# Kernel optimization log

Hardware: AMD Instinct MI355X
Metric: run time of the kernel (lower is better)

The kernel has to match this reference:

```python
import jax, jax.numpy as jnp
import numpy as np

LMAX = 3
MUL = 64


def _build_masks(lmax, mul):
    dim = mul * sum(2 * l + 1 for l in range(lmax + 1))
    masks = np.zeros((lmax + 1, dim), dtype=bool)
    off = 0
    for l in range(lmax + 1):
        base = off + np.arange(mul) * (2 * l + 1) + l
        masks[0, base] = True
        for m in range(1, l + 1):
            masks[m, base + m] = True
            masks[m, base - m] = True
        off += mul * (2 * l + 1)
    idx = [np.nonzero(masks[m])[0] for m in range(lmax + 1)]
    return dim, idx

DIM, IDX = _build_masks(LMAX, MUL)
C_M = [MUL * (LMAX + 1 - m) for m in range(LMAX + 1)]  # 256,192,128,64
WSL = np.cumsum([0] + C_M)  # weight slices per m; weight_numel = 640


def setup_inputs() -> dict:
    E = 65536
    key = jax.random.key(0)
    ks = jax.random.split(key, 16)
    inp = {
        'x': jax.random.normal(ks[0], (E, DIM), jnp.float32),
        'D0': jax.random.normal(ks[1], (E, 1, 1), jnp.float32),
        'D1': jax.random.normal(ks[2], (E, 3, 3), jnp.float32),
        'D2': jax.random.normal(ks[3], (E, 5, 5), jnp.float32),
        'D3': jax.random.normal(ks[4], (E, 7, 7), jnp.float32),
        'weight': jax.random.normal(ks[5], (E, int(WSL[-1])), jnp.float32),
        'mask_edge': jax.random.randint(ks[6], (E,), 0, 2) > 0,
        'W0': jax.random.normal(ks[7], (C_M[0], C_M[0]), jnp.float32) * 0.05,
        'b0': jax.random.normal(ks[8], (C_M[0],), jnp.float32) * 0.05,
        'W1': jax.random.normal(ks[9], (2 * C_M[1], C_M[1]), jnp.float32) * 0.05,
        'W2': jax.random.normal(ks[10], (2 * C_M[2], C_M[2]), jnp.float32) * 0.05,
        'W3': jax.random.normal(ks[11], (2 * C_M[3], C_M[3]), jnp.float32) * 0.05,
    }
    return inp


def _rotate(v, Ds, inverse):
    # per-l block Wigner rotation: [E, mul*(2l+1)] blocks, small batched einsum
    off = 0
    outs = []
    for l in range(LMAX + 1):
        n = 2 * l + 1
        blk = v[:, off:off + MUL * n].reshape(-1, MUL, n)
        if inverse:
            r = jnp.einsum('zcj,zij->zci', blk, Ds[l])
        else:
            r = jnp.einsum('zcj,zji->zci', blk, Ds[l])
        outs.append(r.reshape(-1, MUL * n))
        off += MUL * n
    return jnp.concatenate(outs, axis=-1)


def _so2_forward(x, Ds, weight, mask_edge, W0, b0, Wms):
    x_new = _rotate(x, Ds, inverse=False)
    me = mask_edge.astype(x.dtype)[:, None]
    out = jnp.zeros_like(x_new)  # irreps_out == irreps_in -> same dim
    # m = 0
    x0 = x_new[:, IDX[0]]
    y0 = x0 @ W0.T + b0
    out = out.at[:, IDX[0]].set(y0 * weight[:, WSL[0]:WSL[1]] * me)
    # m > 0
    for m in range(1, LMAX + 1):
        c = C_M[m]
        # gather interleaved (neg, pos) pairs -> [E, 2, c_in]
        xm = x_new[:, IDX[m]].reshape(-1, c, 2).transpose(0, 2, 1)
        y = jnp.einsum('zmc,oc->zmo', xm, Wms[m - 1])  # [E, 2, 2c]
        y_neg = y[:, 0, :c] + y[:, 1, c:]
        y_pos = y[:, 1, :c] - y[:, 0, c:]
        wm = weight[:, WSL[m]:WSL[m + 1]]
        # torch code flattens [neg_all, pos_all] onto ascending masked positions
        vals = jnp.concatenate([y_neg * wm, y_pos * wm], axis=-1) * me
        out = out.at[:, IDX[m]].set(vals)
    return _rotate(out, Ds, inverse=True)


def reference(x, D0, D1, D2, D3, weight, mask_edge, W0, b0, W1, W2, W3):
    return _so2_forward(x, [D0, D1, D2, D3], weight, mask_edge, W0, b0, [W1, W2, W3])
```

## Files before the change

kernel.cpp:

```cpp
#include <hip/hip_runtime.h>
#include <hip/hip_bf16.h>


#define EPB 16
#define BRICK_USHORTS 294912
#define WS_NEED (589824 + 16)

typedef __attribute__((ext_vector_type(8))) short short8v;
typedef __attribute__((ext_vector_type(4))) float float4v;
typedef unsigned short ushort;

__device__ __forceinline__ float bf2f(__hip_bfloat16 v) { return __bfloat162float(v); }
__device__ __forceinline__ ushort f2bb(float v) {
    __hip_bfloat16 h = __float2bfloat16(v);
    return *reinterpret_cast<ushort*>(&h);
}
__device__ __forceinline__ float bb2f(ushort u) {
    __hip_bfloat16 h = *reinterpret_cast<__hip_bfloat16*>(&u);
    return __bfloat162float(h);
}

__device__ int classify_wave(const void* p, int lane)
{
    const unsigned char* b = (const unsigned char*)p;
    bool ok01 = true;
    #pragma unroll
    for (int j = 0; j < 4; ++j) if (b[lane * 4 + j] > 1) ok01 = false;
    if (__all(ok01)) return 0;
    const unsigned* w = (const unsigned*)p;
    const unsigned v = w[lane];
    const unsigned lo = v & 0xFFFFu, hi = v >> 16;
    const bool f32b  = (v == 0u || v == 0x3F800000u);
    const bool bf16b = (lo == 0u || lo == 0x3F80u) && (hi == 0u || hi == 0x3F80u);
    const bool f16b  = (lo == 0u || lo == 0x3C00u) && (hi == 0u || hi == 0x3C00u);
    if (__all(f32b) | __all(bf16b) | __all(f16b)) return 0;
    const float* f = (const float*)p;
    float mx = 0.f;
    #pragma unroll
    for (int j = 0; j < 4; ++j) mx = fmaxf(mx, fabsf(f[lane * 4 + j]));
    #pragma unroll
    for (int d = 1; d < 64; d <<= 1) mx = fmaxf(mx, __shfl_xor(mx, d));
    return (mx < 0.35f) ? 1 : 2;
}

__device__ int detect_stride_wave(const unsigned char* mb, int lane)
{
    unsigned orr[8] = {0,0,0,0,0,0,0,0};
    unsigned maxb = 0, minnz = 255;
    #pragma unroll
    for (int j = 0; j < 16; ++j) {
        unsigned v = mb[lane * 16 + j];
        orr[j & 7] |= v;
        if (v) { maxb = max(maxb, v); minnz = min(minnz, v); }
    }
    #pragma unroll
    for (int d = 1; d < 64; d <<= 1) {
        #pragma unroll
        for (int r = 0; r < 8; ++r) orr[r] |= (unsigned)__shfl_xor((int)orr[r], d);
        maxb  = max(maxb, (unsigned)__shfl_xor((int)maxb, d));
        minnz = min(minnz, (unsigned)__shfl_xor((int)minnz, d));
    }
    const unsigned oddnz = orr[1] | orr[3] | orr[5] | orr[7];
    const bool intbool = (maxb <= 1u) || (maxb == 255u && minnz == 255u);
    if (intbool) {
        if (oddnz)                  return 1;
        else if (orr[2] | orr[6])   return 2;
        else if (orr[4])            return 4;
        else                        return 8;
    } else {
        if (orr[0])                 return 2;
        else if (orr[1])            return 2;
        else if (orr[2])            return 4;
        else                        return 8;
    }
}

__global__ void so2_prep(const void* t0, const void* t1, const void* t2,
                         const float* __restrict__ W1,
                         const float* __restrict__ W2,
                         const float* __restrict__ W3,
                         ushort* __restrict__ Bb)
{
    const int lane = threadIdx.x;
    const int c0 = classify_wave(t0, lane);
    const int c1 = classify_wave(t1, lane);
    const int c2 = classify_wave(t2, lane);
    const void* sel[3];
    int im, id;
    if (c0 != c1 && c0 != c2 && c1 != c2) {
        sel[c0] = t0; sel[c1] = t1; sel[c2] = t2;
        im = (c0 == 0) ? 0 : (c1 == 0) ? 1 : 2;
        id = (c0 == 2) ? 0 : (c1 == 2) ? 1 : 2;
    } else {
        sel[2] = t0; sel[0] = t1; sel[1] = t2;
        im = 1; id = 0;
    }
    const float* sW0 = (const float*)sel[1];
    if (blockIdx.x == 0) {
        const int stride = detect_stride_wave((const unsigned char*)sel[0], lane);
        if (lane == 0) {
            int* hdr = (int*)(Bb + BRICK_USHORTS);
            hdr[0] = im; hdr[1] = id; hdr[2] = stride;
        }
    }

    const int brick = blockIdx.x;
    int m, r, KT;
    if (brick < 128)      { m = 0; r = brick;       KT = 8;  }
    else if (brick < 416) { m = 1; r = brick - 128; KT = 12; }
    else if (brick < 544) { m = 2; r = brick - 416; KT = 8;  }
    else                  { m = 3; r = brick - 544; KT = 4;  }
    const int nt = r / KT, kt = r - nt * KT;
    const float* Wm = (m == 0) ? sW0 : (m == 1) ? W1 : (m == 2) ? W2 : W3;
    const int c = (m == 0) ? 256 : (m == 1) ? 192 : (m == 2) ? 128 : 64;

    const int col = nt * 16 + (lane & 15);
    const int kb  = kt * 32 + (lane >> 4) * 8;
    ushort* dst = Bb + ((size_t)brick << 9) + lane * 8;
    #pragma unroll
    for (int i = 0; i < 8; ++i) {
        const int k = kb + i;
        float v;
        if (m == 0) v = Wm[(size_t)col * 256 + k];
        else if (col < c) v = (k < c) ? Wm[(size_t)col * c + k]
                                      : Wm[(size_t)(c + col) * c + (k - c)];
        else {
            const int o = col - c;
            v = (k < c) ? -Wm[(size_t)(c + o) * c + k]
                        :  Wm[(size_t)o * c + (k - c)];
        }
        dst[i] = f2bb(v);
    }
}

template<int M>
__device__ __forceinline__ void run_unit(
    const ushort (*A_lds)[1024], ushort (*Y_lds)[1024],
    const ushort* __restrict__ Bb,
    const float* __restrict__ weightp, const float* __restrict__ b0,
    const float* me_sh, int e0, int nt, int lane)
{
    constexpr int KT   = (M == 0) ? 8 : (M == 1) ? 12 : (M == 2) ? 8 : 4;
    constexpr int segk = (M == 0) ? 0 : (M == 1) ? 256 : (M == 2) ? 640 : 896;
    constexpr int c    = (M == 0) ? 256 : (M == 1) ? 192 : (M == 2) ? 128 : 64;
    constexpr int wsl  = (M == 0) ? 0 : (M == 1) ? 256 : (M == 2) ? 448 : 576;
    constexpr int bb   = (M == 0) ? 0 : (M == 1) ? 128 : (M == 2) ? 416 : 544;

    const int row16 = lane & 15;
    const int kg    = lane >> 4;
    const int sw    = (row16 & 7) << 3;

    const ushort* bp = Bb + (((size_t)(bb + nt * KT)) << 9) + lane * 8;
    short8v bv[KT];
    #pragma unroll
    for (int kt = 0; kt < KT; ++kt)
        bv[kt] = *(const short8v*)(bp + (size_t)kt * 512);

    float4v acc = {0.f, 0.f, 0.f, 0.f};
    const int k0 = segk + kg * 8;
    #pragma unroll
    for (int kt = 0; kt < KT; ++kt) {
        short8v av = *(const short8v*)&A_lds[row16][(k0 + kt * 32) ^ sw];
        acc = __builtin_amdgcn_mfma_f32_16x16x32_bf16(av, bv[kt], acc, 0, 0, 0);
    }

    const int j  = nt * 16 + row16;
    const int wo = (j < c) ? j : j - c;
    int tgt;
    if (M == 0) { const int l = j >> 6, ch = j & 63; tgt = 64*l*l + l + ch*(2*l+1); }
    else {
        const int p = j >> 1, s = j & 1;
        const int l = M + (p >> 6), ch = p & 63;
        tgt = 64*l*l + l + ch*(2*l+1) + (s ? M : -M);
    }
    const float bias = (M == 0) ? b0[j] : 0.f;
    #pragma unroll
    for (int r = 0; r < 4; ++r) {
        const int e = kg * 4 + r;
        float wgt = 0.f;
        if (me_sh[e] != 0.f)
            wgt = weightp[(size_t)(e0 + e) * 640 + wsl + wo];
        Y_lds[e][tgt] = f2bb((acc[r] + bias) * wgt);
    }
}

__launch_bounds__(512, 2)
__global__ void so2_mfma(const float* __restrict__ x,
                         const void* __restrict__ t0,
                         const void* __restrict__ t1,
                         const void* __restrict__ t2,
                         const float* __restrict__ D1p,
                         const float* __restrict__ D2p,
                         const float* __restrict__ D3p,
                         const float* __restrict__ weightp,
                         const float* __restrict__ b0,
                         const ushort* __restrict__ Bb,
                         float* __restrict__ out)
{
    __shared__ ushort A_lds[EPB][1024];
    __shared__ ushort Y_lds[EPB][1024];
    __shared__ float Dsh[EPB][84];
    __shared__ float me_sh[EPB];
    __shared__ int   mm_sh;
    __shared__ const void*  sel_mask;
    __shared__ const float* sel_D0;

    const int tid  = threadIdx.x;
    const int e0   = blockIdx.x * EPB;
    const int w    = tid >> 6;
    const int lane = tid & 63;

    if (tid == 0) {
        const int* hdr = (const int*)(Bb + BRICK_USHORTS);
        const void* tarr[3] = {t0, t1, t2};
        sel_mask = tarr[hdr[0]];
        sel_D0   = (const float*)tarr[hdr[1]];
        mm_sh    = hdr[2];
    }
    __syncthreads();

    const float* D0p   = sel_D0;
    const void*  maskp = sel_mask;

    for (int idx = tid; idx < EPB * 84; idx += 512) {
        int le = idx / 84, d = idx - le * 84;
        int e = e0 + le;
        float v;
        if (d == 0)      v = D0p[e];
        else if (d < 10) v = D1p[e * 9  + (d - 1)];
        else if (d < 35) v = D2p[e * 25 + (d - 10)];
        else             v = D3p[e * 49 + (d - 35)];
        Dsh[le][d] = v;
    }
    if (tid >= 64 && tid < 64 + EPB) {
        const int le = tid - 64;
        const int stride = mm_sh;
        const size_t e = (size_t)e0 + le;
        int mv;
        if (stride == 1)      mv = ((const unsigned char*)maskp)[e]      != 0;
        else if (stride == 2) mv = ((const unsigned short*)maskp)[e]     != 0;
        else if (stride == 4) mv = ((const unsigned int*)maskp)[e]       != 0u;
        else                  mv = ((const unsigned long long*)maskp)[e] != 0ULL;
        me_sh[le] = mv ? 1.0f : 0.0f;
    }
    __syncthreads();

    {
        float (*XF)[1024] = reinterpret_cast<float(*)[1024]>(Y_lds);
        float4 rx[2][4];
        bool live[2];
        #pragma unroll
        for (int s = 0; s < 2; ++s) {
            const int e = s * 8 + w;
            live[s] = (me_sh[e] != 0.0f);
            if (live[s]) {
                const float4* src = (const float4*)(x + (size_t)(e0 + e) * 1024);
                #pragma unroll
                for (int t = 0; t < 4; ++t) rx[s][t] = src[lane + t * 64];
            }
        }
        #pragma unroll
        for (int s = 0; s < 2; ++s) {
            const int e  = s * 8 + w;
            const int sw = (e & 7) << 3;
            if (!live[s]) {
                const short8v z = {0,0,0,0,0,0,0,0};
                *(short8v*)&A_lds[e][lane * 16]     = z;
                *(short8v*)&A_lds[e][lane * 16 + 8] = z;
                continue;
            }
            float4* dst = (float4*)XF[w];
            #pragma unroll
            for (int t = 0; t < 4; ++t) dst[lane + t * 64] = rx[s][t];
            const float* xr = XF[w];
            const int ch = lane;
            A_lds[e][ch ^ sw] = f2bb(xr[ch] * Dsh[e][0]);
            #pragma unroll
            for (int l = 1; l <= 3; ++l) {
                const int n   = 2 * l + 1;
                const int off = 64 * l * l;
                const int odl = (l == 1) ? 1 : (l == 2) ? 10 : 35;
                float xv[7];
                #pragma unroll
                for (int j = 0; j < n; ++j) xv[j] = xr[off + ch * n + j];
                #pragma unroll
                for (int i = 0; i < n; ++i) {
                    float v = 0.f;
                    #pragma unroll
                    for (int j = 0; j < n; ++j) v += xv[j] * Dsh[e][odl + j * n + i];
                    int col;
                    if (i == l) col = l * 64 + ch;
                    else if (i < l) {
                        const int m = l - i;
                        const int segb = (m == 1) ? 256 : (m == 2) ? 640 : 896;
                        col = segb + i * 64 + ch;
                    } else {
                        const int m = i - l;
                        const int segb = (m == 1) ? 256 : (m == 2) ? 640 : 896;
                        const int cs   = (m == 1) ? 192 : (m == 2) ? 128 : 64;
                        col = segb + cs + (2 * l - i) * 64 + ch;
                    }
                    A_lds[e][col ^ sw] = f2bb(v);
                }
            }
        }
    }
    __syncthreads();

    {
        run_unit<0>(A_lds, Y_lds, Bb, weightp, b0, me_sh, e0, w,      lane);
        run_unit<0>(A_lds, Y_lds, Bb, weightp, b0, me_sh, e0, w + 8,  lane);
        run_unit<1>(A_lds, Y_lds, Bb, weightp, b0, me_sh, e0, w,      lane);
        run_unit<1>(A_lds, Y_lds, Bb, weightp, b0, me_sh, e0, w + 8,  lane);
        run_unit<1>(A_lds, Y_lds, Bb, weightp, b0, me_sh, e0, w + 16, lane);
        run_unit<2>(A_lds, Y_lds, Bb, weightp, b0, me_sh, e0, w,      lane);
        run_unit<2>(A_lds, Y_lds, Bb, weightp, b0, me_sh, e0, w + 8,  lane);
        run_unit<3>(A_lds, Y_lds, Bb, weightp, b0, me_sh, e0, w,      lane);
    }
    __syncthreads();

    {
        float (*OF)[1024] = reinterpret_cast<float(*)[1024]>(A_lds);
        #pragma unroll
        for (int s = 0; s < 2; ++s) {
            const int e = s * 8 + w;
            float4* dst = (float4*)(out + (size_t)(e0 + e) * 1024);
            if (me_sh[e] == 0.0f) {
                float4 z; z.x = z.y = z.z = z.w = 0.f;
                #pragma unroll
                for (int t = 0; t < 4; ++t) dst[lane + t * 64] = z;
                continue;
            }
            const int ch = lane;
            OF[w][ch] = bb2f(Y_lds[e][ch]) * Dsh[e][0];
            #pragma unroll
            for (int l = 1; l <= 3; ++l) {
                const int n   = 2 * l + 1;
                const int off = 64 * l * l;
                const int odl = (l == 1) ? 1 : (l == 2) ? 10 : 35;
                float yv[7];
                #pragma unroll
                for (int j = 0; j < n; ++j) yv[j] = bb2f(Y_lds[e][off + ch * n + j]);
                #pragma unroll
                for (int i = 0; i < n; ++i) {
                    float o = 0.f;
                    #pragma unroll
                    for (int j = 0; j < n; ++j) o += yv[j] * Dsh[e][odl + i * n + j];
                    OF[w][off + ch * n + i] = o;
                }
            }
            const float4* srcv = (const float4*)OF[w];
            #pragma unroll
            for (int t = 0; t < 4; ++t) dst[lane + t * 64] = srcv[lane + t * 64];
        }
    }
}

__device__ int classify_buf(const void* p)
{
    const unsigned char* b = (const unsigned char*)p;
    bool bytes01 = true;
    for (int i = 0; i < 256; ++i) if (b[i] > 1) { bytes01 = false; break; }
    if (bytes01) return 0;
    const unsigned* w = (const unsigned*)p;
    bool f32b = true, bf16b = true, f16b = true;
    for (int i = 0; i < 64; ++i) {
        unsigned v = w[i];
        if (v != 0u && v != 0x3F800000u) f32b = false;
        unsigned lo = v & 0xFFFFu, hi = v >> 16;
        if (!((lo == 0u || lo == 0x3F80u) && (hi == 0u || hi == 0x3F80u))) bf16b = false;
        if (!((lo == 0u || lo == 0x3C00u) && (hi == 0u || hi == 0x3C00u))) f16b = false;
    }
    if (f32b | bf16b | f16b) return 0;
    const float* f = (const float*)p;
    float mx = 0.f;
    for (int i = 0; i < 256; ++i) { float a = fabsf(f[i]); if (a > mx) mx = a; }
    return (mx < 0.35f) ? 1 : 2;
}

__device__ int detect_stride(const unsigned char* mb)
{
    unsigned or8[8] = {0,0,0,0,0,0,0,0};
    unsigned maxb = 0, minnz = 255;
    for (int i = 0; i < 1024; ++i) {
        unsigned v = mb[i];
        or8[i & 7] |= v;
        if (v) { if (v > maxb) maxb = v; if (v < minnz) minnz = v; }
    }
    const unsigned oddnz = or8[1] | or8[3] | or8[5] | or8[7];
    const bool intbool = (maxb <= 1u) || (maxb == 255u && minnz == 255u);
    if (intbool) {
        if (oddnz)                return 1;
        else if (or8[2] | or8[6]) return 2;
        else if (or8[4])          return 4;
        else                      return 8;
    } else {
        if (or8[0])               return 2;
        else if (or8[1])          return 2;
        else if (or8[2])          return 4;
        else                      return 8;
    }
}

template<int M>
__device__ void seg_m(const __hip_bfloat16 XN[1024][9], int le,
                      const float* __restrict__ Wm, int j0, float* val)
{
    constexpr int C = 64 * (4 - M);
    const bool side = (j0 < C);
    const float* w1 = Wm + (size_t)j0 * C;
    const float* w2 = Wm + (size_t)(side ? j0 + C : j0 - C) * C;
    float acc0[16], acc1[16];
    #pragma unroll
    for (int u = 0; u < 16; ++u) { acc0[u] = 0.f; acc1[u] = 0.f; }
    #pragma unroll
    for (int lq = 0; lq <= 3 - M; ++lq) {
        const int l = M + lq, n = 2 * l + 1;
        const int a0 = 64 * l * l + l;
        for (int ch = 0; ch < 64; ch += 4) {
            const int b0_ = a0 + (ch + 0) * n, b1_ = a0 + (ch + 1) * n;
            const int b2_ = a0 + (ch + 2) * n, b3_ = a0 + (ch + 3) * n;
            const float xn0 = bf2f(XN[b0_ - M][le]), xp0 = bf2f(XN[b0_ + M][le]);
            const float xn1 = bf2f(XN[b1_ - M][le]), xp1 = bf2f(XN[b1_ + M][le]);
            const float xn2 = bf2f(XN[b2_ - M][le]), xp2 = bf2f(XN[b2_ + M][le]);
            const float xn3 = bf2f(XN[b3_ - M][le]), xp3 = bf2f(XN[b3_ + M][le]);
            const int p = lq * 64 + ch;
            #pragma unroll
            for (int u = 0; u < 16; ++u) {
                const float4 w1v = *(const float4*)(w1 + u * C + p);
                acc0[u] += xn0 * w1v.x + xn1 * w1v.y + xn2 * w1v.z + xn3 * w1v.w;
                const float4 w2v = *(const float4*)(w2 + u * C + p);
                acc1[u] += xp0 * w2v.x + xp1 * w2v.y + xp2 * w2v.z + xp3 * w2v.w;
            }
        }
    }
    #pragma unroll
    for (int u = 0; u < 16; ++u) val[u] = (side ? acc0[u] : -acc0[u]) + acc1[u];
}

__device__ void seg_m0(const __hip_bfloat16 XN[1024][9], int le,
                       const float* __restrict__ W0, const float* __restrict__ b0,
                       int j0, float* val)
{
    const float* w = W0 + (size_t)j0 * 256;
    float acc[16];
    #pragma unroll
    for (int u = 0; u < 16; ++u) acc[u] = 0.f;
    #pragma unroll
    for (int l = 0; l < 4; ++l) {
        const int n = 2 * l + 1, a0 = 64 * l * l + l;
        for (int ch = 0; ch < 64; ch += 4) {
            const float x0 = bf2f(XN[a0 + (ch + 0) * n][le]);
            const float x1 = bf2f(XN[a0 + (ch + 1) * n][le]);
            const float x2 = bf2f(XN[a0 + (ch + 2) * n][le]);
            const float x3 = bf2f(XN[a0 + (ch + 3) * n][le]);
            const int k = l * 64 + ch;
            #pragma unroll
            for (int u = 0; u < 16; ++u) {
                const float4 wv = *(const float4*)(w + u * 256 + k);
                acc[u] += x0 * wv.x + x1 * wv.y + x2 * wv.z + x3 * wv.w;
            }
        }
    }
    #pragma unroll
    for (int u = 0; u < 16; ++u) val[u] = acc[u] + b0[j0 + u];
}

__launch_bounds__(512)
__global__ void so2_scalar(const float* __restrict__ x,
                           const void* __restrict__ t0,
                           const void* __restrict__ t1,
                           const void* __restrict__ t2,
                           const float* __restrict__ D1p,
                           const float* __restrict__ D2p,
                           const float* __restrict__ D3p,
                           const float* __restrict__ weightp,
                           const float* __restrict__ b0,
                           const float* __restrict__ W1,
                           const float* __restrict__ W2,
                           const float* __restrict__ W3,
                           float* __restrict__ out)
{
    __shared__ __hip_bfloat16 XN[1024][9];
    __shared__ __hip_bfloat16 ON[1024][9];
    __shared__ float Dsh[8][84];
    __shared__ float me_sh[8];
    __shared__ int   mm_sh;
    __shared__ const void*  sel_mask;
    __shared__ const float* sel_W0;
    __shared__ const float* sel_D0;

    const int tid = threadIdx.x;
    const int e0  = blockIdx.x * 8;

    if (tid == 0) {
        int c0 = classify_buf(t0), c1 = classify_buf(t1), c2 = classify_buf(t2);
        const void* sel[3];
        if (c0 != c1 && c0 != c2 && c1 != c2) { sel[c0] = t0; sel[c1] = t1; sel[c2] = t2; }
        else { sel[2] = t0; sel[0] = t1; sel[1] = t2; }
        sel_mask = sel[0];
        sel_W0   = (const float*)sel[1];
        sel_D0   = (const float*)sel[2];
        mm_sh = detect_stride((const unsigned char*)sel[0]);
    }
    __syncthreads();

    const float* D0p   = sel_D0;
    const float* W0    = sel_W0;
    const void*  maskp = sel_mask;

    for (int idx = tid; idx < 8 * 84; idx += 512) {
        int le = idx / 84, d = idx - le * 84;
        int e = e0 + le;
        float v;
        if (d == 0)      v = D0p[e];
        else if (d < 10) v = D1p[e * 9  + (d - 1)];
        else if (d < 35) v = D2p[e * 25 + (d - 10)];
        else             v = D3p[e * 49 + (d - 35)];
        Dsh[le][d] = v;
    }
    if (tid >= 64 && tid < 72) {
        const int le = tid - 64;
        const int stride = mm_sh;
        const size_t e = (size_t)e0 + le;
        int mv;
        if (stride == 1)      mv = ((const unsigned char*)maskp)[e]      != 0;
        else if (stride == 2) mv = ((const unsigned short*)maskp)[e]     != 0;
        else if (stride == 4) mv = ((const unsigned int*)maskp)[e]       != 0u;
        else                  mv = ((const unsigned long long*)maskp)[e] != 0ULL;
        me_sh[le] = mv ? 1.0f : 0.0f;
    }
    __syncthreads();

    {
        const int le = tid >> 6;
        const int ch = tid & 63;
        const float* xr = x + (size_t)(e0 + le) * 1024;
        XN[ch][le] = __float2bfloat16(xr[ch] * Dsh[le][0]);
        #pragma unroll
        for (int l = 1; l <= 3; ++l) {
            const int n   = 2 * l + 1;
            const int off = 64 * l * l;
            const int odl = (l == 1) ? 1 : (l == 2) ? 10 : 35;
            float xv[7];
            #pragma unroll
            for (int j = 0; j < n; ++j) xv[j] = xr[off + ch * n + j];
            #pragma unroll
            for (int i = 0; i < n; ++i) {
                float v = 0.f;
                #pragma unroll
                for (int j = 0; j < n; ++j) v += xv[j] * Dsh[le][odl + j * n + i];
                XN[off + ch * n + i][le] = __float2bfloat16(v);
            }
        }
    }
    __syncthreads();

    {
        const int g  = tid >> 3;
        const int le = tid & 7;
        const float mew = me_sh[le];
        const float* wrow = weightp + (size_t)(e0 + le) * 640;
        float val[16];
        int m, j0, c, wsl;
        if (g < 16)      { m = 0; j0 = g * 16;        c = 256; wsl = 0;   }
        else if (g < 40) { m = 1; j0 = (g - 16) * 16; c = 192; wsl = 256; }
        else if (g < 56) { m = 2; j0 = (g - 40) * 16; c = 128; wsl = 448; }
        else             { m = 3; j0 = (g - 56) * 16; c = 64;  wsl = 576; }

        if      (m == 0) seg_m0(XN, le, W0, b0, j0, val);
        else if (m == 1) seg_m<1>(XN, le, W1, j0, val);
        else if (m == 2) seg_m<2>(XN, le, W2, j0, val);
        else             seg_m<3>(XN, le, W3, j0, val);

        #pragma unroll
        for (int u = 0; u < 16; ++u) {
            const int j  = j0 + u;
            const int wo = (j < c) ? j : j - c;
            const float v = val[u] * wrow[wsl + wo] * mew;
            int tgt;
            if (m == 0) { const int l = j >> 6, ch = j & 63; tgt = 64 * l * l + l + ch * (2 * l + 1); }
            else {
                const int p = j >> 1, s = j & 1;
                const int l = m + (p >> 6), ch = p & 63;
                tgt = 64 * l * l + l + ch * (2 * l + 1) + (s ? m : -m);
            }
            ON[tgt][le] = __float2bfloat16(v);
        }
    }
    __syncthreads();

    {
        const int le = tid >> 6;
        const int ch = tid & 63;
        float* orow = out + (size_t)(e0 + le) * 1024;
        orow[ch] = bf2f(ON[ch][le]) * Dsh[le][0];
        #pragma unroll
        for (int l = 1; l <= 3; ++l) {
            const int n   = 2 * l + 1;
            const int off = 64 * l * l;
            const int odl = (l == 1) ? 1 : (l == 2) ? 10 : 35;
            float yv[7];
            #pragma unroll
            for (int j = 0; j < n; ++j) yv[j] = bf2f(ON[off + ch * n + j][le]);
            #pragma unroll
            for (int i = 0; i < n; ++i) {
                float o = 0.f;
                #pragma unroll
                for (int j = 0; j < n; ++j) o += yv[j] * Dsh[le][odl + i * n + j];
                orow[off + ch * n + i] = o;
            }
        }
    }
}

extern "C" void kernel_launch(void* const* d_in, const int* in_sizes, int n_in,
                              void* d_out, int out_size, void* d_ws, size_t ws_size,
                              hipStream_t stream)
{
    const float *x = nullptr, *D1p = nullptr, *D2p = nullptr, *D3p = nullptr;
    const float *weight = nullptr, *b0 = nullptr, *W1 = nullptr, *W2 = nullptr, *W3 = nullptr;
    const void* trio[3] = {nullptr, nullptr, nullptr};
    int nt = 0;
    bool ok = (n_in == 12);
    if (ok) {
        for (int i = 0; i < 12; ++i) {
            switch (in_sizes[i]) {
                case 67108864: x      = (const float*)d_in[i]; break;
                case 589824:   D1p    = (const float*)d_in[i]; break;
                case 1638400:  D2p    = (const float*)d_in[i]; break;
                case 3211264:  D3p    = (const float*)d_in[i]; break;
                case 41943040: weight = (const float*)d_in[i]; break;
                case 256:      b0     = (const float*)d_in[i]; break;
                case 73728:    W1     = (const float*)d_in[i]; break;
                case 32768:    W2     = (const float*)d_in[i]; break;
                case 8192:     W3     = (const float*)d_in[i]; break;
                case 65536:    if (nt < 3) trio[nt++] = d_in[i]; break;
                default: break;
            }
        }
        ok = x && D1p && D2p && D3p && weight && b0 && W1 && W2 && W3 && (nt == 3);
    }
    if (!ok) {
        x      = (const float*)d_in[0];
        trio[0] = d_in[1];
        D1p    = (const float*)d_in[2];
        D2p    = (const float*)d_in[3];
        D3p    = (const float*)d_in[4];
        weight = (const float*)d_in[5];
        trio[1] = d_in[6];
        trio[2] = d_in[7];
        b0     = (const float*)d_in[8];
        W1     = (const float*)d_in[9];
        W2     = (const float*)d_in[10];
        W3     = (const float*)d_in[11];
    }
    float* out = (float*)d_out;
    const int E = out_size / 1024;

    if (ws_size >= (size_t)WS_NEED) {
        ushort* Bb = (ushort*)d_ws;
        so2_prep<<<576, 64, 0, stream>>>(trio[0], trio[1], trio[2], W1, W2, W3, Bb);
        so2_mfma<<<E / EPB, 512, 0, stream>>>(x, trio[0], trio[1], trio[2],
                                              D1p, D2p, D3p, weight, b0, Bb, out);
    } else {
        so2_scalar<<<E / 8, 512, 0, stream>>>(x, trio[0], trio[1], trio[2],
                                              D1p, D2p, D3p, weight,
                                              b0, W1, W2, W3, out);
    }

    hipError_t lerr = hipGetLastError();
    if (lerr != hipSuccess) {
        unsigned char pat = (unsigned char)(0x60 | ((unsigned)lerr & 0xF));
        hipMemsetAsync(d_out, pat, (size_t)out_size * 4, stream);
    }
}
```

Baseline: 328.9 us.

## Halve edges per block to 8 and raise occupancy with bf16 LDS staging

Cuts edges per block from 16 to 8 and raises launch bounds from 2 to 8 blocks per CU, so each wave handles one edge. The MFMA tiles run with half the rows zeroed, and B loads are chunked in groups of four to reduce register pressure. Input x is staged in LDS as bf16 instead of fp32, and the output rotation is split into two phases that reuse a small per-wave fp32 buffer. The aim is more resident waves to hide memory latency, at the cost of half-wasted MFMA work, extra bf16 rounding of the input, and more B-matrix reloads per edge.

```diff
diff --git a/kernel.cpp b/kernel.cpp
--- a/kernel.cpp
+++ b/kernel.cpp
@@ -2,7 +2,7 @@
 #include <hip/hip_bf16.h>
 
 
-#define EPB 16
+#define EPB 8
 #define BRICK_USHORTS 294912
 #define WS_NEED (589824 + 16)
 
@@ -148,43 +148,50 @@
 
     const int row16 = lane & 15;
     const int kg    = lane >> 4;
-    const int sw    = (row16 & 7) << 3;
+    const bool arow = row16 < 8;
+    const int  row  = row16 & 7;
+    const int  sw   = row << 3;
 
     const ushort* bp = Bb + (((size_t)(bb + nt * KT)) << 9) + lane * 8;
-    short8v bv[KT];
-    #pragma unroll
-    for (int kt = 0; kt < KT; ++kt)
-        bv[kt] = *(const short8v*)(bp + (size_t)kt * 512);
-
+    const int k0 = segk + kg * 8;
     float4v acc = {0.f, 0.f, 0.f, 0.f};
-    const int k0 = segk + kg * 8;
-    #pragma unroll
-    for (int kt = 0; kt < KT; ++kt) {
-        short8v av = *(const short8v*)&A_lds[row16][(k0 + kt * 32) ^ sw];
-        acc = __builtin_amdgcn_mfma_f32_16x16x32_bf16(av, bv[kt], acc, 0, 0, 0);
-    }
-
-    const int j  = nt * 16 + row16;
-    const int wo = (j < c) ? j : j - c;
-    int tgt;
-    if (M == 0) { const int l = j >> 6, ch = j & 63; tgt = 64*l*l + l + ch*(2*l+1); }
-    else {
-        const int p = j >> 1, s = j & 1;
-        const int l = M + (p >> 6), ch = p & 63;
-        tgt = 64*l*l + l + ch*(2*l+1) + (s ? M : -M);
-    }
-    const float bias = (M == 0) ? b0[j] : 0.f;
-    #pragma unroll
-    for (int r = 0; r < 4; ++r) {
-        const int e = kg * 4 + r;
-        float wgt = 0.f;
-        if (me_sh[e] != 0.f)
-            wgt = weightp[(size_t)(e0 + e) * 640 + wsl + wo];
-        Y_lds[e][tgt] = f2bb((acc[r] + bias) * wgt);
-    }
-}
-
-__launch_bounds__(512, 2)
+    const short8v z8 = {0,0,0,0,0,0,0,0};
+
+    #pragma unroll
+    for (int kc = 0; kc < KT; kc += 4) {
+        short8v bv[4];
+        #pragma unroll
+        for (int q = 0; q < 4; ++q)
+            bv[q] = *(const short8v*)(bp + (size_t)(kc + q) * 512);
+        #pragma unroll
+        for (int q = 0; q < 4; ++q) {
+            short8v av = *(const short8v*)&A_lds[row][(k0 + (kc + q) * 32) ^ sw];
+            av = arow ? av : z8;
+            acc = __builtin_amdgcn_mfma_f32_16x16x32_bf16(av, bv[q], acc, 0, 0, 0);
+        }
+    }
+
+    if (kg < 2) {
+        const int j  = nt * 16 + row16;
+        const int wo = (j < c) ? j : j - c;
+        int tgt;
+        if (M == 0) { const int l = j >> 6, ch = j & 63; tgt = 64*l*l + l + ch*(2*l+1); }
+        else {
+            const int p = j >> 1, s = j & 1;
+            const int l = M + (p >> 6), ch = p & 63;
+            tgt = 64*l*l + l + ch*(2*l+1) + (s ? M : -M);
+        }
+        const float bias = (M == 0) ? b0[j] : 0.f;
+        #pragma unroll
+        for (int r = 0; r < 4; ++r) {
+            const int e = kg * 4 + r;
+            const float wgt = weightp[(size_t)(e0 + e) * 640 + wsl + wo] * me_sh[e];
+            Y_lds[e][tgt] = f2bb((acc[r] + bias) * wgt);
+        }
+    }
+}
+
+__launch_bounds__(512, 8)
 __global__ void so2_mfma(const float* __restrict__ x,
                          const void* __restrict__ t0,
                          const void* __restrict__ t1,
@@ -198,7 +205,7 @@
                          float* __restrict__ out)
 {
     __shared__ ushort A_lds[EPB][1024];
-    __shared__ ushort Y_lds[EPB][1024];
+    __shared__ ushort YX[EPB][1024];
     __shared__ float Dsh[EPB][84];
     __shared__ float me_sh[EPB];
     __shared__ int   mm_sh;
@@ -246,35 +253,25 @@
     __syncthreads();
 
     {
-        float (*XF)[1024] = reinterpret_cast<float(*)[1024]>(Y_lds);
-        float4 rx[2][4];
-        bool live[2];
-        #pragma unroll
-        for (int s = 0; s < 2; ++s) {
-            const int e = s * 8 + w;
-            live[s] = (me_sh[e] != 0.0f);
-            if (live[s]) {
-                const float4* src = (const float4*)(x + (size_t)(e0 + e) * 1024);
-                #pragma unroll
-                for (int t = 0; t < 4; ++t) rx[s][t] = src[lane + t * 64];
-            }
-        }
-        #pragma unroll
-        for (int s = 0; s < 2; ++s) {
-            const int e  = s * 8 + w;
-            const int sw = (e & 7) << 3;
-            if (!live[s]) {
-                const short8v z = {0,0,0,0,0,0,0,0};
-                *(short8v*)&A_lds[e][lane * 16]     = z;
-                *(short8v*)&A_lds[e][lane * 16 + 8] = z;
-                continue;
-            }
-            float4* dst = (float4*)XF[w];
-            #pragma unroll
-            for (int t = 0; t < 4; ++t) dst[lane + t * 64] = rx[s][t];
-            const float* xr = XF[w];
+        const int e = w;
+        const int sw = e << 3;
+        if (me_sh[e] == 0.0f) {
+            const short8v z = {0,0,0,0,0,0,0,0};
+            *(short8v*)&A_lds[e][lane * 16]     = z;
+            *(short8v*)&A_lds[e][lane * 16 + 8] = z;
+        } else {
+            const float4* src = (const float4*)(x + (size_t)(e0 + e) * 1024);
+            #pragma unroll
+            for (int t = 0; t < 4; ++t) {
+                const float4 v = src[lane + t * 64];
+                uint2 u;
+                u.x = (unsigned)f2bb(v.x) | ((unsigned)f2bb(v.y) << 16);
+                u.y = (unsigned)f2bb(v.z) | ((unsigned)f2bb(v.w) << 16);
+                *(uint2*)&YX[e][4 * (lane + t * 64)] = u;
+            }
+            const ushort* xr = YX[e];
             const int ch = lane;
-            A_lds[e][ch ^ sw] = f2bb(xr[ch] * Dsh[e][0]);
+            A_lds[e][ch ^ sw] = f2bb(bb2f(xr[ch]) * Dsh[e][0]);
             #pragma unroll
             for (int l = 1; l <= 3; ++l) {
                 const int n   = 2 * l + 1;
@@ -282,7 +279,7 @@
                 const int odl = (l == 1) ? 1 : (l == 2) ? 10 : 35;
                 float xv[7];
                 #pragma unroll
-                for (int j = 0; j < n; ++j) xv[j] = xr[off + ch * n + j];
+                for (int j = 0; j < n; ++j) xv[j] = bb2f(xr[off + ch * n + j]);
                 #pragma unroll
                 for (int i = 0; i < n; ++i) {
                     float v = 0.f;
@@ -308,50 +305,82 @@
     __syncthreads();
 
     {
-        run_unit<0>(A_lds, Y_lds, Bb, weightp, b0, me_sh, e0, w,      lane);
-        run_unit<0>(A_lds, Y_lds, Bb, weightp, b0, me_sh, e0, w + 8,  lane);
-        run_unit<1>(A_lds, Y_lds, Bb, weightp, b0, me_sh, e0, w,      lane);
-        run_unit<1>(A_lds, Y_lds, Bb, weightp, b0, me_sh, e0, w + 8,  lane);
-        run_unit<1>(A_lds, Y_lds, Bb, weightp, b0, me_sh, e0, w + 16, lane);
-        run_unit<2>(A_lds, Y_lds, Bb, weightp, b0, me_sh, e0, w,      lane);
-        run_unit<2>(A_lds, Y_lds, Bb, weightp, b0, me_sh, e0, w + 8,  lane);
-        run_unit<3>(A_lds, Y_lds, Bb, weightp, b0, me_sh, e0, w,      lane);
+        run_unit<0>(A_lds, YX, Bb, weightp, b0, me_sh, e0, w,      lane);
+        run_unit<0>(A_lds, YX, Bb, weightp, b0, me_sh, e0, w + 8,  lane);
+        run_unit<1>(A_lds, YX, Bb, weightp, b0, me_sh, e0, w,      lane);
+        run_unit<1>(A_lds, YX, Bb, weightp, b0, me_sh, e0, w + 8,  lane);
+        run_unit<1>(A_lds, YX, Bb, weightp, b0, me_sh, e0, w + 16, lane);
+        run_unit<2>(A_lds, YX, Bb, weightp, b0, me_sh, e0, w,      lane);
+        run_unit<2>(A_lds, YX, Bb, weightp, b0, me_sh, e0, w + 8,  lane);
+        run_unit<3>(A_lds, YX, Bb, weightp, b0, me_sh, e0, w,      lane);
     }
     __syncthreads();
 
     {
-        float (*OF)[1024] = reinterpret_cast<float(*)[1024]>(A_lds);
-        #pragma unroll
-        for (int s = 0; s < 2; ++s) {
-            const int e = s * 8 + w;
-            float4* dst = (float4*)(out + (size_t)(e0 + e) * 1024);
-            if (me_sh[e] == 0.0f) {
-                float4 z; z.x = z.y = z.z = z.w = 0.f;
-                #pragma unroll
-                for (int t = 0; t < 4; ++t) dst[lane + t * 64] = z;
-                continue;
-            }
+        const int e = w;
+        float* orow = out + (size_t)(e0 + e) * 1024;
+        if (me_sh[e] == 0.0f) {
+            float4 z; z.x = z.y = z.z = z.w = 0.f;
+            float4* dst = (float4*)orow;
+            #pragma unroll
+            for (int t = 0; t < 4; ++t) dst[lane + t * 64] = z;
+        } else {
+            float* OFw = (float*)&A_lds[w][0];
+            const ushort* yr = YX[e];
             const int ch = lane;
-            OF[w][ch] = bb2f(Y_lds[e][ch]) * Dsh[e][0];
-            #pragma unroll
-            for (int l = 1; l <= 3; ++l) {
-                const int n   = 2 * l + 1;
-                const int off = 64 * l * l;
-                const int odl = (l == 1) ? 1 : (l == 2) ? 10 : 35;
+            OFw[ch] = bb2f(yr[ch]) * Dsh[e][0];
+            {
                 float yv[7];
                 #pragma unroll
-                for (int j = 0; j < n; ++j) yv[j] = bb2f(Y_lds[e][off + ch * n + j]);
-                #pragma unroll
-                for (int i = 0; i < n; ++i) {
+                for (int j = 0; j < 7; ++j) yv[j] = bb2f(yr[576 + ch * 7 + j]);
+                #pragma unroll
+                for (int i = 0; i < 7; ++i) {
                     float o = 0.f;
                     #pragma unroll
-                    for (int j = 0; j < n; ++j) o += yv[j] * Dsh[e][odl + i * n + j];
-                    OF[w][off + ch * n + i] = o;
+                    for (int j = 0; j < 7; ++j) o += yv[j] * Dsh[e][35 + i * 7 + j];
+                    OFw[64 + ch * 7 + i] = o;
                 }
             }
-            const float4* srcv = (const float4*)OF[w];
-            #pragma unroll
-            for (int t = 0; t < 4; ++t) dst[lane + t * 64] = srcv[lane + t * 64];
+            {
+                const float4* OF4 = (const float4*)OFw;
+                #pragma unroll
+                for (int t = 0; t < 2; ++t) {
+                    const int k = lane + t * 64;
+                    const float4 v = OF4[k];
+                    float* d = (k < 16) ? (orow + 4 * k) : (orow + 512 + 4 * k);
+                    *(float4*)d = v;
+                }
+            }
+            {
+                float yv[3];
+                #pragma unroll
+                for (int j = 0; j < 3; ++j) yv[j] = bb2f(yr[64 + ch * 3 + j]);
+                #pragma unroll
+                for (int i = 0; i < 3; ++i) {
+                    float o = 0.f;
+                    #pragma unroll
+                    for (int j = 0; j < 3; ++j) o += yv[j] * Dsh[e][1 + i * 3 + j];
+                    OFw[ch * 3 + i] = o;
+                }
+                float yv2[5];
+                #pragma unroll
+                for (int j = 0; j < 5; ++j) yv2[j] = bb2f(yr[256 + ch * 5 + j]);
+                #pragma unroll
+                for (int i = 0; i < 5; ++i) {
+                    float o = 0.f;
+                    #pragma unroll
+                    for (int j = 0; j < 5; ++j) o += yv2[j] * Dsh[e][10 + i * 5 + j];
+                    OFw[192 + ch * 5 + i] = o;
+                }
+            }
+            {
+                const float4* OF4 = (const float4*)OFw;
+                #pragma unroll
+                for (int t = 0; t < 2; ++t) {
+                    const int k = lane + t * 64;
+                    *(float4*)(orow + 64 + 4 * k) = OF4[k];
+                }
+            }
         }
     }
 }
```

New measurement: 528.7 us. 60.8% more time.
